# Optimization experiments

Hardware: AMD Instinct MI355X
Metric: run time of the kernel (lower is better)

## Reference

```python
import jax, jax.numpy as jnp
import numpy as np
import math

B, N, HW, D, H = 4, 1024, 4096, 512, 8
DK = D // H
EPS = 0.1


def setup_inputs() -> dict:
    key = jax.random.key(0)
    ks = jax.random.split(key, 12)
    s = 1.0 / math.sqrt(D)
    query = jax.random.normal(ks[0], (B, N, D), dtype=jnp.float32)
    key_t = jax.random.normal(ks[1], (B, HW, D), dtype=jnp.float32)
    value = jax.random.normal(ks[2], (B, HW, D), dtype=jnp.float32)
    # 2D spatial positions of the feature map in [0,1]^2
    x_tilde = jax.random.uniform(ks[3], (HW, 2), dtype=jnp.float32)
    # predicted positions per query: close to x_tilde so each row has unmasked keys
    x_hat = x_tilde[None, :, :] + 0.1 * jax.random.normal(ks[4], (N, HW, 2), dtype=jnp.float32)
    Wq = jax.random.normal(ks[5], (D, D), dtype=jnp.float32) * s
    Wk = jax.random.normal(ks[6], (D, D), dtype=jnp.float32) * s
    Wv = jax.random.normal(ks[7], (D, D), dtype=jnp.float32) * s
    Wo = jax.random.normal(ks[8], (D, D), dtype=jnp.float32) * s
    bq = jnp.zeros((D,), jnp.float32)
    bk = jnp.zeros((D,), jnp.float32)
    bv = jnp.zeros((D,), jnp.float32)
    bo = jnp.zeros((D,), jnp.float32)
    return {"query": query, "key": key_t, "value": value,
            "x_tilde": x_tilde, "x_hat": x_hat,
            "Wq": Wq, "bq": bq, "Wk": Wk, "bk": bk,
            "Wv": Wv, "bv": bv, "Wo": Wo, "bo": bo}


def reference(query, key, value, x_tilde, x_hat, Wq, bq, Wk, bk, Wv, bv, Wo, bo):
    b, n, d = query.shape
    hw = key.shape[1]
    # nn.Linear: x @ W^T + b
    Q = (query @ Wq.T + bq).reshape(b, n, H, DK).transpose(0, 2, 1, 3)   # [B,H,N,DK]
    K = (key @ Wk.T + bk).reshape(b, hw, H, DK).transpose(0, 2, 1, 3)    # [B,H,HW,DK]
    V = (value @ Wv.T + bv).reshape(b, hw, H, DK).transpose(0, 2, 1, 3)  # [B,H,HW,DK]
    scores = jnp.einsum('bhnd,bhmd->bhnm', Q, K) / math.sqrt(DK)         # [B,H,N,HW]
    # geometric mask: 0 where ||x_tilde_j - x_hat_ij|| < eps else -inf
    dist = jnp.linalg.norm(x_tilde[None, :, :] - x_hat, axis=-1)         # [N,HW]
    m_geo = jnp.where(dist < EPS, 0.0, -jnp.inf).astype(scores.dtype)
    scores = scores + m_geo[None, None, :, :]
    attn = jax.nn.softmax(scores, axis=-1)                               # [B,H,N,HW]
    # dropout is identity in eval mode
    ctx = jnp.einsum('bhnm,bhmd->bhnd', attn, V)                         # [B,H,N,DK]
    ctx = ctx.transpose(0, 2, 1, 3).reshape(b, n, d)
    out = ctx @ Wo.T + bo
    return (out, attn)
```

## Files before the change

kernel.cpp:

```cpp
#include <hip/hip_runtime.h>
#include <math.h>

typedef _Float16 h8 __attribute__((ext_vector_type(8)));
typedef _Float16 h4 __attribute__((ext_vector_type(4)));
typedef float    f4 __attribute__((ext_vector_type(4)));

#define NQ    1024
#define HWK   4096
#define DM    512
#define NH    8
#define DKH   64

__global__ __launch_bounds__(256)
void cvt_f16_kernel(const float* __restrict__ in, _Float16* __restrict__ out, int n8)
{
    int i = blockIdx.x * blockDim.x + threadIdx.x;
    if (i >= n8) return;
    const f4* q = (const f4*)(in + (size_t)i * 8);
    f4 a = __builtin_nontemporal_load(q);
    f4 b = __builtin_nontemporal_load(q + 1);
    h8 r;
    r[0] = (_Float16)a[0]; r[1] = (_Float16)a[1];
    r[2] = (_Float16)a[2]; r[3] = (_Float16)a[3];
    r[4] = (_Float16)b[0]; r[5] = (_Float16)b[1];
    r[6] = (_Float16)b[2]; r[7] = (_Float16)b[3];
    *(h8*)(out + (size_t)i * 8) = r;
}

__global__ __launch_bounds__(256)
void mask_kernel(const float* __restrict__ x_tilde, const float* __restrict__ x_hat,
                 _Float16* __restrict__ maskT)
{
    __shared__ _Float16 T[64][72];
    int t  = threadIdx.x;
    int jl = t & 63;
    int iw = t >> 6;
    int j0 = blockIdx.x * 64;
    int i0 = blockIdx.y * 64;

    float xt0 = x_tilde[(j0 + jl) * 2 + 0];
    float xt1 = x_tilde[(j0 + jl) * 2 + 1];

    for (int ii = iw; ii < 64; ii += 4) {
        size_t idx = ((size_t)(i0 + ii) * HWK + j0 + jl) * 2;
        float h0 = __builtin_nontemporal_load(x_hat + idx + 0);
        float h1 = __builtin_nontemporal_load(x_hat + idx + 1);
        float dx = xt0 - h0, dy = xt1 - h1;
        float d2 = __fadd_rn(__fmul_rn(dx, dx), __fmul_rn(dy, dy));
        float dist = __fsqrt_rn(d2);
        T[ii][jl] = (dist < 0.1f) ? (_Float16)0.0f : (_Float16)(-__builtin_inff());
    }
    __syncthreads();
    int il = t & 63;
    for (int jj = iw; jj < 64; jj += 4) {
        maskT[(size_t)(j0 + jj) * NQ + i0 + il] = T[il][jj];
    }
}

__global__ __launch_bounds__(256)
void proj_qk(const _Float16* __restrict__ X, const _Float16* __restrict__ W,
             const float* __restrict__ bias, _Float16* __restrict__ out,
             int nlog2, float scale)
{
    int tid = threadIdx.x;
    int w = tid >> 6, lane = tid & 63, q = lane >> 4, c = lane & 15;
    int wr = blockIdx.x * 128 + (w >> 1) * 64;
    int wc = blockIdx.y * 128 + (w & 1) * 64;

    f4 acc[4][4];
    const f4 fz = {0.f, 0.f, 0.f, 0.f};
#pragma unroll
    for (int i = 0; i < 4; i++)
#pragma unroll
        for (int j = 0; j < 4; j++) acc[i][j] = fz;

    for (int k0 = 0; k0 < DM; k0 += 32) {
        h8 af[4], bf[4];
#pragma unroll
        for (int i = 0; i < 4; i++)
            af[i] = *(const h8*)(X + (size_t)(wr + i * 16 + c) * DM + k0 + q * 8);
#pragma unroll
        for (int j = 0; j < 4; j++)
            bf[j] = *(const h8*)(W + (size_t)(wc + j * 16 + c) * DM + k0 + q * 8);
#pragma unroll
        for (int i = 0; i < 4; i++)
#pragma unroll
            for (int j = 0; j < 4; j++)
                acc[i][j] = __builtin_amdgcn_mfma_f32_16x16x32_f16(af[i], bf[j], acc[i][j], 0, 0, 0);
    }

    int nmask = (1 << nlog2) - 1;
#pragma unroll
    for (int j = 0; j < 4; j++) {
        int ncol = wc + j * 16 + c;
        float bb = bias[ncol];
        int hh = ncol >> 6, dk = ncol & 63;
#pragma unroll
        for (int i = 0; i < 4; i++) {
#pragma unroll
            for (int r = 0; r < 4; r++) {
                int m = wr + i * 16 + q * 4 + r;
                int b = m >> nlog2, n = m & nmask;
                float v = (acc[i][j][r] + bb) * scale;
                out[((((size_t)(b * NH + hh)) << nlog2) + n) * DKH + dk] = (_Float16)v;
            }
        }
    }
}

__global__ __launch_bounds__(256)
void proj_v(const _Float16* __restrict__ V, const _Float16* __restrict__ W,
            const float* __restrict__ bias, _Float16* __restrict__ out)
{
    int tid = threadIdx.x;
    int w = tid >> 6, lane = tid & 63, q = lane >> 4, c = lane & 15;
    int wr = blockIdx.x * 128 + (w >> 1) * 64;
    int wc = blockIdx.y * 128 + (w & 1) * 64;

    f4 acc[4][4];
    const f4 fz = {0.f, 0.f, 0.f, 0.f};
#pragma unroll
    for (int i = 0; i < 4; i++)
#pragma unroll
        for (int j = 0; j < 4; j++) acc[i][j] = fz;

    for (int k0 = 0; k0 < DM; k0 += 32) {
        h8 af[4], bf[4];
#pragma unroll
        for (int i = 0; i < 4; i++)
            af[i] = *(const h8*)(W + (size_t)(wr + i * 16 + c) * DM + k0 + q * 8);
#pragma unroll
        for (int j = 0; j < 4; j++)
            bf[j] = *(const h8*)(V + (size_t)(wc + j * 16 + c) * DM + k0 + q * 8);
#pragma unroll
        for (int i = 0; i < 4; i++)
#pragma unroll
            for (int j = 0; j < 4; j++)
                acc[i][j] = __builtin_amdgcn_mfma_f32_16x16x32_f16(af[i], bf[j], acc[i][j], 0, 0, 0);
    }

#pragma unroll
    for (int i = 0; i < 4; i++) {
#pragma unroll
        for (int r = 0; r < 4; r++) {
            int f = wr + i * 16 + q * 4 + r;
            float bb = bias[f];
            int hh = f >> 6, dk = f & 63;
#pragma unroll
            for (int j = 0; j < 4; j++) {
                int col = wc + j * 16 + c;
                int b = col >> 12, hw = col & 4095;
                out[((size_t)(b * NH + hh) * DKH + dk) * HWK + hw] =
                    (_Float16)(acc[i][j][r] + bb);
            }
        }
    }
}

__global__ __launch_bounds__(256)
void proj_o(const _Float16* __restrict__ C, const _Float16* __restrict__ W,
            const float* __restrict__ bias, float* __restrict__ out)
{
    int tid = threadIdx.x;
    int w = tid >> 6, lane = tid & 63, q = lane >> 4, c = lane & 15;
    int wr = blockIdx.x * 128 + (w >> 1) * 64;
    int wc = blockIdx.y * 128 + (w & 1) * 64;

    f4 acc[4][4];
    const f4 fz = {0.f, 0.f, 0.f, 0.f};
#pragma unroll
    for (int i = 0; i < 4; i++)
#pragma unroll
        for (int j = 0; j < 4; j++) acc[i][j] = fz;

    for (int k0 = 0; k0 < DM; k0 += 32) {
        h8 af[4], bf[4];
#pragma unroll
        for (int i = 0; i < 4; i++)
            af[i] = *(const h8*)(C + (size_t)(wr + i * 16 + c) * DM + k0 + q * 8);
#pragma unroll
        for (int j = 0; j < 4; j++)
            bf[j] = *(const h8*)(W + (size_t)(wc + j * 16 + c) * DM + k0 + q * 8);
#pragma unroll
        for (int i = 0; i < 4; i++)
#pragma unroll
            for (int j = 0; j < 4; j++)
                acc[i][j] = __builtin_amdgcn_mfma_f32_16x16x32_f16(af[i], bf[j], acc[i][j], 0, 0, 0);
    }

#pragma unroll
    for (int j = 0; j < 4; j++) {
        int ncol = wc + j * 16 + c;
        float bb = bias[ncol];
#pragma unroll
        for (int i = 0; i < 4; i++) {
#pragma unroll
            for (int r = 0; r < 4; r++) {
                int m = wr + i * 16 + q * 4 + r;
                __builtin_nontemporal_store(acc[i][j][r] + bb, &out[(size_t)m * DM + ncol]);
            }
        }
    }
}

__global__ __launch_bounds__(256)
void attn_kernel(const _Float16* __restrict__ Qh, const _Float16* __restrict__ Kh,
                 const _Float16* __restrict__ Vt, const _Float16* __restrict__ maskT,
                 float* __restrict__ attn_out, _Float16* __restrict__ ctx_h)
{
    __shared__ union SmU {
        _Float16 P[4][32][68];
        float    C[32][68];
    } sm;
    __shared__ float red[4][32];
    __shared__ float invl[32];

    int tid = threadIdx.x;
    int w = tid >> 6, lane = tid & 63, q = lane >> 4, c = lane & 15;
    int bh = blockIdx.x >> 5;
    int n0 = (blockIdx.x & 31) * 32;
    int b = bh >> 3, h = bh & 7;

    const _Float16* Qb = Qh + ((size_t)bh * NQ + n0) * DKH;
    const _Float16* Kb = Kh + (size_t)bh * HWK * DKH;
    const _Float16* Vb = Vt + (size_t)bh * DKH * HWK;
    float* attn_b = attn_out + ((size_t)bh * NQ + n0) * HWK;

    h8 qa[2][2];
#pragma unroll
    for (int i = 0; i < 2; i++)
#pragma unroll
        for (int ks = 0; ks < 2; ks++)
            qa[i][ks] = *(const h8*)(Qb + (size_t)(i * 16 + c) * DKH + ks * 32 + q * 8);

    float lsum[2][4];
#pragma unroll
    for (int i = 0; i < 2; i++)
#pragma unroll
        for (int r = 0; r < 4; r++) lsum[i][r] = 0.f;

    for (int it = 0; it < 16; ++it) {
        int m0 = it * 256 + w * 64;
        h8 kb[4][2];
#pragma unroll
        for (int j = 0; j < 4; j++)
#pragma unroll
            for (int ks = 0; ks < 2; ks++)
                kb[j][ks] = *(const h8*)(Kb + (size_t)(m0 + j * 16 + c) * DKH + ks * 32 + q * 8);
#pragma unroll
        for (int i = 0; i < 2; i++) {
#pragma unroll
            for (int j = 0; j < 4; j++) {
                f4 acc = {0.f, 0.f, 0.f, 0.f};
                __builtin_amdgcn_s_setprio(1);
                acc = __builtin_amdgcn_mfma_f32_16x16x32_f16(qa[i][0], kb[j][0], acc, 0, 0, 0);
                acc = __builtin_amdgcn_mfma_f32_16x16x32_f16(qa[i][1], kb[j][1], acc, 0, 0, 0);
                __builtin_amdgcn_s_setprio(0);
                h4 mk = *(const h4*)(maskT + (size_t)(m0 + j * 16 + c) * NQ + n0 + i * 16 + q * 4);
#pragma unroll
                for (int r = 0; r < 4; r++)
                    lsum[i][r] += __expf(acc[r] + (float)mk[r]);
            }
        }
    }

#pragma unroll
    for (int i = 0; i < 2; i++) {
#pragma unroll
        for (int r = 0; r < 4; r++) {
            float s = lsum[i][r];
            s += __shfl_xor(s, 1);
            s += __shfl_xor(s, 2);
            s += __shfl_xor(s, 4);
            s += __shfl_xor(s, 8);
            if (c == 0) red[w][i * 16 + q * 4 + r] = s;
        }
    }
    __syncthreads();
    if (tid < 32)
        invl[tid] = 1.0f / (red[0][tid] + red[1][tid] + red[2][tid] + red[3][tid]);
    __syncthreads();

    f4 cacc[2][4];
    const f4 fz = {0.f, 0.f, 0.f, 0.f};
#pragma unroll
    for (int i = 0; i < 2; i++)
#pragma unroll
        for (int jd = 0; jd < 4; jd++) cacc[i][jd] = fz;

    for (int it = 0; it < 16; ++it) {
        int m0 = it * 256 + w * 64;
        h8 kb[4][2];
#pragma unroll
        for (int j = 0; j < 4; j++)
#pragma unroll
            for (int ks = 0; ks < 2; ks++)
                kb[j][ks] = *(const h8*)(Kb + (size_t)(m0 + j * 16 + c) * DKH + ks * 32 + q * 8);

#pragma unroll
        for (int i = 0; i < 2; i++) {
#pragma unroll
            for (int j = 0; j < 4; j++) {
                f4 acc = {0.f, 0.f, 0.f, 0.f};
                __builtin_amdgcn_s_setprio(1);
                acc = __builtin_amdgcn_mfma_f32_16x16x32_f16(qa[i][0], kb[j][0], acc, 0, 0, 0);
                acc = __builtin_amdgcn_mfma_f32_16x16x32_f16(qa[i][1], kb[j][1], acc, 0, 0, 0);
                __builtin_amdgcn_s_setprio(0);
                h4 mk = *(const h4*)(maskT + (size_t)(m0 + j * 16 + c) * NQ + n0 + i * 16 + q * 4);
#pragma unroll
                for (int r = 0; r < 4; r++) {
                    float e = __expf(acc[r] + (float)mk[r]);
                    sm.P[w][i * 16 + q * 4 + r][j * 16 + c] = (_Float16)e;
                }
            }
        }
#pragma unroll
        for (int ks = 0; ks < 2; ks++) {
            h8 pa[2], vb[4];
#pragma unroll
            for (int i = 0; i < 2; i++)
                pa[i] = *(const h8*)&sm.P[w][i * 16 + c][ks * 32 + q * 8];
#pragma unroll
            for (int jd = 0; jd < 4; jd++)
                vb[jd] = *(const h8*)(Vb + (size_t)(jd * 16 + c) * HWK + m0 + ks * 32 + q * 8);
            __builtin_amdgcn_s_setprio(1);
#pragma unroll
            for (int i = 0; i < 2; i++)
#pragma unroll
                for (int jd = 0; jd < 4; jd++)
                    cacc[i][jd] = __builtin_amdgcn_mfma_f32_16x16x32_f16(pa[i], vb[jd], cacc[i][jd], 0, 0, 0);
            __builtin_amdgcn_s_setprio(0);
        }
#pragma unroll
        for (int r0 = 0; r0 < 32; r0 += 4) {
            int row = r0 + q;
            h4 pv = *(const h4*)&sm.P[w][row][c * 4];
            float il = invl[row];
            f4 o;
            o[0] = (float)pv[0] * il;
            o[1] = (float)pv[1] * il;
            o[2] = (float)pv[2] * il;
            o[3] = (float)pv[3] * il;
            __builtin_nontemporal_store(o, (f4*)(attn_b + (size_t)row * HWK + m0 + c * 4));
        }
    }

    __syncthreads();
    for (int idx = tid; idx < 32 * 68; idx += 256)
        (&sm.C[0][0])[idx] = 0.f;
    __syncthreads();
#pragma unroll
    for (int i = 0; i < 2; i++)
#pragma unroll
        for (int jd = 0; jd < 4; jd++)
#pragma unroll
            for (int r = 0; r < 4; r++)
                atomicAdd(&sm.C[i * 16 + q * 4 + r][jd * 16 + c], cacc[i][jd][r]);
    __syncthreads();

    _Float16* ctx_b = ctx_h + ((size_t)b * NQ + n0) * DM + h * DKH;
    for (int r0 = 0; r0 < 32; r0 += 4) {
        int row = r0 + w;
        int col = tid & 63;
        float v = sm.C[row][col] * invl[row];
        ctx_b[(size_t)row * DM + col] = (_Float16)v;
    }
}

extern "C" void kernel_launch(void* const* d_in, const int* in_sizes, int n_in,
                              void* d_out, int out_size, void* d_ws, size_t ws_size,
                              hipStream_t stream)
{
    const float* query   = (const float*)d_in[0];
    const float* key     = (const float*)d_in[1];
    const float* value   = (const float*)d_in[2];
    const float* x_tilde = (const float*)d_in[3];
    const float* x_hat   = (const float*)d_in[4];
    const float* Wq = (const float*)d_in[5];
    const float* bq = (const float*)d_in[6];
    const float* Wk = (const float*)d_in[7];
    const float* bk = (const float*)d_in[8];
    const float* Wv = (const float*)d_in[9];
    const float* bv = (const float*)d_in[10];
    const float* Wo = (const float*)d_in[11];
    const float* bo = (const float*)d_in[12];

    char* ws = (char*)d_ws;
    _Float16* Qh    = (_Float16*)(ws);
    _Float16* Kh    = (_Float16*)(ws + ((size_t)4  << 20));
    _Float16* Vt    = (_Float16*)(ws + ((size_t)20 << 20));
    _Float16* ctxh  = (_Float16*)(ws + ((size_t)36 << 20));
    _Float16* maskT = (_Float16*)(ws + ((size_t)40 << 20));
    _Float16* Xq    = (_Float16*)(ws + ((size_t)48 << 20));
    _Float16* Xk    = (_Float16*)(ws + ((size_t)52 << 20));
    _Float16* Xv    = (_Float16*)(ws + ((size_t)68 << 20));
    _Float16* Wqh   = (_Float16*)(ws + ((size_t)84 << 20));
    _Float16* Wkh   = (_Float16*)(ws + ((size_t)84 << 20) + (512 * 1024));
    _Float16* Wvh   = (_Float16*)(ws + ((size_t)84 << 20) + (1024 * 1024));
    _Float16* Woh   = (_Float16*)(ws + ((size_t)84 << 20) + (1536 * 1024));

    float* out  = (float*)d_out;
    float* attn = out + (size_t)4 * NQ * DM;

    const int NW8 = DM * DM / 8;
    cvt_f16_kernel<<<(4 * NQ * DM / 8 + 255) / 256, 256, 0, stream>>>(query, Xq, 4 * NQ * DM / 8);
    cvt_f16_kernel<<<(4 * HWK * DM / 8 + 255) / 256, 256, 0, stream>>>(key, Xk, 4 * HWK * DM / 8);
    cvt_f16_kernel<<<(4 * HWK * DM / 8 + 255) / 256, 256, 0, stream>>>(value, Xv, 4 * HWK * DM / 8);
    cvt_f16_kernel<<<(NW8 + 255) / 256, 256, 0, stream>>>(Wq, Wqh, NW8);
    cvt_f16_kernel<<<(NW8 + 255) / 256, 256, 0, stream>>>(Wk, Wkh, NW8);
    cvt_f16_kernel<<<(NW8 + 255) / 256, 256, 0, stream>>>(Wv, Wvh, NW8);
    cvt_f16_kernel<<<(NW8 + 255) / 256, 256, 0, stream>>>(Wo, Woh, NW8);

    mask_kernel<<<dim3(HWK / 64, NQ / 64), 256, 0, stream>>>(x_tilde, x_hat, maskT);
    proj_qk<<<dim3(4 * NQ / 128, DM / 128), 256, 0, stream>>>(Xq, Wqh, bq, Qh, 10, 0.125f);
    proj_qk<<<dim3(4 * HWK / 128, DM / 128), 256, 0, stream>>>(Xk, Wkh, bk, Kh, 12, 1.0f);
    proj_v<<<dim3(DM / 128, 4 * HWK / 128), 256, 0, stream>>>(Xv, Wvh, bv, Vt);
    attn_kernel<<<32 * (NQ / 32), 256, 0, stream>>>(Qh, Kh, Vt, maskT, attn, ctxh);
    proj_o<<<dim3(4 * NQ / 128, DM / 128), 256, 0, stream>>>(ctxh, Woh, bo, out);
}
```

Measured before the change: 1.006 ms.

## Swap MFMA operands to keep mask untransposed and write attn directly

Swaps the operand order of the score MFMAs so each lane holds four consecutive key columns of one query row. This lets the mask be stored in natural [N,HW] layout, which the mask kernel now writes with vector stores and no shared-memory transpose. The normalized attention probabilities are written straight from registers, dropping the separate LDS re-read loop, and the row-sum reduction now needs fewer shuffles. The change also swizzles the block index so neighbouring blocks share query tiles across heads, and removes the s_setprio hints. The attn stores now go out as 16-byte pieces per lane scattered across 16 rows, which may coalesce worse.

```diff
diff --git a/kernel.cpp b/kernel.cpp
--- a/kernel.cpp
+++ b/kernel.cpp
@@ -29,32 +29,25 @@
 
 __global__ __launch_bounds__(256)
 void mask_kernel(const float* __restrict__ x_tilde, const float* __restrict__ x_hat,
-                 _Float16* __restrict__ maskT)
-{
-    __shared__ _Float16 T[64][72];
-    int t  = threadIdx.x;
-    int jl = t & 63;
-    int iw = t >> 6;
-    int j0 = blockIdx.x * 64;
-    int i0 = blockIdx.y * 64;
-
-    float xt0 = x_tilde[(j0 + jl) * 2 + 0];
-    float xt1 = x_tilde[(j0 + jl) * 2 + 1];
-
-    for (int ii = iw; ii < 64; ii += 4) {
-        size_t idx = ((size_t)(i0 + ii) * HWK + j0 + jl) * 2;
-        float h0 = __builtin_nontemporal_load(x_hat + idx + 0);
-        float h1 = __builtin_nontemporal_load(x_hat + idx + 1);
-        float dx = xt0 - h0, dy = xt1 - h1;
+                 _Float16* __restrict__ mask)
+{
+    int idx = blockIdx.x * 256 + threadIdx.x;
+    int n   = idx >> 9;
+    int kv0 = (idx & 511) * 8;
+
+    const float* xh = x_hat + ((size_t)n * HWK + kv0) * 2;
+    const float* xt = x_tilde + (size_t)kv0 * 2;
+    h8 r;
+#pragma unroll
+    for (int t = 0; t < 8; t++) {
+        float h0 = __builtin_nontemporal_load(xh + t * 2 + 0);
+        float h1 = __builtin_nontemporal_load(xh + t * 2 + 1);
+        float dx = xt[t * 2 + 0] - h0, dy = xt[t * 2 + 1] - h1;
         float d2 = __fadd_rn(__fmul_rn(dx, dx), __fmul_rn(dy, dy));
         float dist = __fsqrt_rn(d2);
-        T[ii][jl] = (dist < 0.1f) ? (_Float16)0.0f : (_Float16)(-__builtin_inff());
-    }
-    __syncthreads();
-    int il = t & 63;
-    for (int jj = iw; jj < 64; jj += 4) {
-        maskT[(size_t)(j0 + jj) * NQ + i0 + il] = T[il][jj];
-    }
+        r[t] = (dist < 0.1f) ? (_Float16)0.0f : (_Float16)(-__builtin_inff());
+    }
+    *(h8*)(mask + (size_t)n * HWK + kv0) = r;
 }
 
 __global__ __launch_bounds__(256)
@@ -205,7 +198,7 @@
 
 __global__ __launch_bounds__(256)
 void attn_kernel(const _Float16* __restrict__ Qh, const _Float16* __restrict__ Kh,
-                 const _Float16* __restrict__ Vt, const _Float16* __restrict__ maskT,
+                 const _Float16* __restrict__ Vt, const _Float16* __restrict__ mask,
                  float* __restrict__ attn_out, _Float16* __restrict__ ctx_h)
 {
     __shared__ union SmU {
@@ -217,13 +210,16 @@
 
     int tid = threadIdx.x;
     int w = tid >> 6, lane = tid & 63, q = lane >> 4, c = lane & 15;
-    int bh = blockIdx.x >> 5;
-    int n0 = (blockIdx.x & 31) * 32;
+
+    int swz = ((blockIdx.x & 7) << 7) | (blockIdx.x >> 3);
+    int bh = swz >> 5;
+    int n0 = (swz & 31) * 32;
     int b = bh >> 3, h = bh & 7;
 
     const _Float16* Qb = Qh + ((size_t)bh * NQ + n0) * DKH;
     const _Float16* Kb = Kh + (size_t)bh * HWK * DKH;
     const _Float16* Vb = Vt + (size_t)bh * DKH * HWK;
+    const _Float16* mask_b = mask + (size_t)n0 * HWK;
     float* attn_b = attn_out + ((size_t)bh * NQ + n0) * HWK;
 
     h8 qa[2][2];
@@ -233,11 +229,7 @@
         for (int ks = 0; ks < 2; ks++)
             qa[i][ks] = *(const h8*)(Qb + (size_t)(i * 16 + c) * DKH + ks * 32 + q * 8);
 
-    float lsum[2][4];
-#pragma unroll
-    for (int i = 0; i < 2; i++)
-#pragma unroll
-        for (int r = 0; r < 4; r++) lsum[i][r] = 0.f;
+    float lsum[2] = {0.f, 0.f};
 
     for (int it = 0; it < 16; ++it) {
         int m0 = it * 256 + w * 64;
@@ -252,35 +244,32 @@
 #pragma unroll
             for (int j = 0; j < 4; j++) {
                 f4 acc = {0.f, 0.f, 0.f, 0.f};
-                __builtin_amdgcn_s_setprio(1);
-                acc = __builtin_amdgcn_mfma_f32_16x16x32_f16(qa[i][0], kb[j][0], acc, 0, 0, 0);
-                acc = __builtin_amdgcn_mfma_f32_16x16x32_f16(qa[i][1], kb[j][1], acc, 0, 0, 0);
-                __builtin_amdgcn_s_setprio(0);
-                h4 mk = *(const h4*)(maskT + (size_t)(m0 + j * 16 + c) * NQ + n0 + i * 16 + q * 4);
+                acc = __builtin_amdgcn_mfma_f32_16x16x32_f16(kb[j][0], qa[i][0], acc, 0, 0, 0);
+                acc = __builtin_amdgcn_mfma_f32_16x16x32_f16(kb[j][1], qa[i][1], acc, 0, 0, 0);
+                h4 mk = *(const h4*)(mask_b + (size_t)(i * 16 + c) * HWK + m0 + j * 16 + q * 4);
 #pragma unroll
                 for (int r = 0; r < 4; r++)
-                    lsum[i][r] += __expf(acc[r] + (float)mk[r]);
+                    lsum[i] += __expf(acc[r] + (float)mk[r]);
             }
         }
     }
 
 #pragma unroll
     for (int i = 0; i < 2; i++) {
-#pragma unroll
-        for (int r = 0; r < 4; r++) {
-            float s = lsum[i][r];
-            s += __shfl_xor(s, 1);
-            s += __shfl_xor(s, 2);
-            s += __shfl_xor(s, 4);
-            s += __shfl_xor(s, 8);
-            if (c == 0) red[w][i * 16 + q * 4 + r] = s;
-        }
+        float s = lsum[i];
+        s += __shfl_xor(s, 16);
+        s += __shfl_xor(s, 32);
+        if (q == 0) red[w][i * 16 + c] = s;
     }
     __syncthreads();
     if (tid < 32)
         invl[tid] = 1.0f / (red[0][tid] + red[1][tid] + red[2][tid] + red[3][tid]);
     __syncthreads();
 
+    float il[2];
+#pragma unroll
+    for (int i = 0; i < 2; i++) il[i] = invl[i * 16 + c];
+
     f4 cacc[2][4];
     const f4 fz = {0.f, 0.f, 0.f, 0.f};
 #pragma unroll
@@ -302,16 +291,23 @@
 #pragma unroll
             for (int j = 0; j < 4; j++) {
                 f4 acc = {0.f, 0.f, 0.f, 0.f};
-                __builtin_amdgcn_s_setprio(1);
-                acc = __builtin_amdgcn_mfma_f32_16x16x32_f16(qa[i][0], kb[j][0], acc, 0, 0, 0);
-                acc = __builtin_amdgcn_mfma_f32_16x16x32_f16(qa[i][1], kb[j][1], acc, 0, 0, 0);
-                __builtin_amdgcn_s_setprio(0);
-                h4 mk = *(const h4*)(maskT + (size_t)(m0 + j * 16 + c) * NQ + n0 + i * 16 + q * 4);
-#pragma unroll
-                for (int r = 0; r < 4; r++) {
-                    float e = __expf(acc[r] + (float)mk[r]);
-                    sm.P[w][i * 16 + q * 4 + r][j * 16 + c] = (_Float16)e;
-                }
+                acc = __builtin_amdgcn_mfma_f32_16x16x32_f16(kb[j][0], qa[i][0], acc, 0, 0, 0);
+                acc = __builtin_amdgcn_mfma_f32_16x16x32_f16(kb[j][1], qa[i][1], acc, 0, 0, 0);
+                h4 mk = *(const h4*)(mask_b + (size_t)(i * 16 + c) * HWK + m0 + j * 16 + q * 4);
+                float e0 = __expf(acc[0] + (float)mk[0]);
+                float e1 = __expf(acc[1] + (float)mk[1]);
+                float e2 = __expf(acc[2] + (float)mk[2]);
+                float e3 = __expf(acc[3] + (float)mk[3]);
+                h4 ev;
+                ev[0] = (_Float16)e0; ev[1] = (_Float16)e1;
+                ev[2] = (_Float16)e2; ev[3] = (_Float16)e3;
+                *(h4*)&sm.P[w][i * 16 + c][j * 16 + q * 4] = ev;
+                float s = il[i];
+                f4 o;
+                o[0] = (float)ev[0] * s; o[1] = (float)ev[1] * s;
+                o[2] = (float)ev[2] * s; o[3] = (float)ev[3] * s;
+                __builtin_nontemporal_store(o,
+                    (f4*)(attn_b + (size_t)(i * 16 + c) * HWK + m0 + j * 16 + q * 4));
             }
         }
 #pragma unroll
@@ -323,25 +319,11 @@
 #pragma unroll
             for (int jd = 0; jd < 4; jd++)
                 vb[jd] = *(const h8*)(Vb + (size_t)(jd * 16 + c) * HWK + m0 + ks * 32 + q * 8);
-            __builtin_amdgcn_s_setprio(1);
 #pragma unroll
             for (int i = 0; i < 2; i++)
 #pragma unroll
                 for (int jd = 0; jd < 4; jd++)
                     cacc[i][jd] = __builtin_amdgcn_mfma_f32_16x16x32_f16(pa[i], vb[jd], cacc[i][jd], 0, 0, 0);
-            __builtin_amdgcn_s_setprio(0);
-        }
-#pragma unroll
-        for (int r0 = 0; r0 < 32; r0 += 4) {
-            int row = r0 + q;
-            h4 pv = *(const h4*)&sm.P[w][row][c * 4];
-            float il = invl[row];
-            f4 o;
-            o[0] = (float)pv[0] * il;
-            o[1] = (float)pv[1] * il;
-            o[2] = (float)pv[2] * il;
-            o[3] = (float)pv[3] * il;
-            __builtin_nontemporal_store(o, (f4*)(attn_b + (size_t)row * HWK + m0 + c * 4));
         }
     }
 
@@ -390,7 +372,7 @@
     _Float16* Kh    = (_Float16*)(ws + ((size_t)4  << 20));
     _Float16* Vt    = (_Float16*)(ws + ((size_t)20 << 20));
     _Float16* ctxh  = (_Float16*)(ws + ((size_t)36 << 20));
-    _Float16* maskT = (_Float16*)(ws + ((size_t)40 << 20));
+    _Float16* maskN = (_Float16*)(ws + ((size_t)40 << 20));
     _Float16* Xq    = (_Float16*)(ws + ((size_t)48 << 20));
     _Float16* Xk    = (_Float16*)(ws + ((size_t)52 << 20));
     _Float16* Xv    = (_Float16*)(ws + ((size_t)68 << 20));
@@ -411,10 +393,10 @@
     cvt_f16_kernel<<<(NW8 + 255) / 256, 256, 0, stream>>>(Wv, Wvh, NW8);
     cvt_f16_kernel<<<(NW8 + 255) / 256, 256, 0, stream>>>(Wo, Woh, NW8);
 
-    mask_kernel<<<dim3(HWK / 64, NQ / 64), 256, 0, stream>>>(x_tilde, x_hat, maskT);
+    mask_kernel<<<NQ * HWK / 8 / 256, 256, 0, stream>>>(x_tilde, x_hat, maskN);
     proj_qk<<<dim3(4 * NQ / 128, DM / 128), 256, 0, stream>>>(Xq, Wqh, bq, Qh, 10, 0.125f);
     proj_qk<<<dim3(4 * HWK / 128, DM / 128), 256, 0, stream>>>(Xk, Wkh, bk, Kh, 12, 1.0f);
     proj_v<<<dim3(DM / 128, 4 * HWK / 128), 256, 0, stream>>>(Xv, Wvh, bv, Vt);
-    attn_kernel<<<32 * (NQ / 32), 256, 0, stream>>>(Qh, Kh, Vt, maskT, attn, ctxh);
+    attn_kernel<<<32 * (NQ / 32), 256, 0, stream>>>(Qh, Kh, Vt, maskN, attn, ctxh);
     proj_o<<<dim3(4 * NQ / 128, DM / 128), 256, 0, stream>>>(ctxh, Woh, bo, out);
 }
```

Result: no change. 1.003 ms (-0.2%).
